# Kernel optimization log

Measured on AMD Instinct MI355X. Metric: run time of the kernel, lower is better.

The kernel has to match this reference:

```python
import jax, jax.numpy as jnp
import numpy as np

NUM_HEADS = 16


def setup_inputs() -> dict:
    key = jax.random.key(0)
    ks = jax.random.split(key, 10)
    B, S, D = 2, 2048, 1024
    x = jax.random.normal(ks[0], (B, S, D), dtype=jnp.float32)
    mask = jax.random.randint(ks[1], (B, 1, 1, S), 0, 2, dtype=jnp.int32)
    scale = 1.0 / np.sqrt(D)
    wq = jax.random.normal(ks[2], (D, D), dtype=jnp.float32) * scale
    bq = jnp.zeros((D,), dtype=jnp.float32)
    wk = jax.random.normal(ks[3], (D, D), dtype=jnp.float32) * scale
    bk = jnp.zeros((D,), dtype=jnp.float32)
    wv = jax.random.normal(ks[4], (D, D), dtype=jnp.float32) * scale
    bv = jnp.zeros((D,), dtype=jnp.float32)
    wo = jax.random.normal(ks[5], (D, D), dtype=jnp.float32) * scale
    bo = jnp.zeros((D,), dtype=jnp.float32)
    return {"x": x, "mask": mask, "wq": wq, "bq": bq, "wk": wk, "bk": bk,
            "wv": wv, "bv": bv, "wo": wo, "bo": bo}


def reference(x, mask, wq, bq, wk, bk, wv, bv, wo, bo):
    B, S, D = x.shape
    H = NUM_HEADS
    dk = D // H

    def split_heads(t):
        # (B, S, D) -> (B, H, S, dk)
        return t.reshape(B, S, H, dk).transpose(0, 2, 1, 3)

    # PyTorch nn.Linear: y = x @ W^T + b
    q = split_heads(x @ wq.T + bq)
    k = split_heads(x @ wk.T + bk)
    v = split_heads(x @ wv.T + bv)

    # scaled dot-product attention with explicit score matrix (as original)
    logits = jnp.einsum('bhqd,bhkd->bhqk', q, k) / jnp.sqrt(jnp.float32(dk))
    logits = jnp.where(mask == 0, jnp.float32(-1e9), logits)
    attn_weights = jax.nn.softmax(logits, axis=-1)
    # dropout(p=0.1) is identity in eval mode (deterministic reference)
    attn = jnp.einsum('bhqk,bhkd->bhqd', attn_weights, v)

    attn = attn.transpose(0, 2, 1, 3).reshape(B, S, D)
    out = attn @ wo.T + bo
    return out, attn_weights
```

## Files before the change

kernel.cpp:

```cpp
#include <hip/hip_runtime.h>
#include <hip/hip_bf16.h>

#define DEV __device__ __forceinline__

typedef __attribute__((ext_vector_type(8))) __bf16 bf16x8;
typedef __attribute__((ext_vector_type(8))) short s16x8;
typedef __attribute__((ext_vector_type(4))) float f32x4;
typedef __attribute__((ext_vector_type(2))) unsigned long long u64x2;

DEV f32x4 mfma16(s16x8 a, s16x8 b, f32x4 c){
  return __builtin_amdgcn_mfma_f32_16x16x32_bf16(
      __builtin_bit_cast(bf16x8, a), __builtin_bit_cast(bf16x8, b), c, 0, 0, 0);
}

DEV unsigned int cvtpk(float a, float b){
  float2 t; t.x = a; t.y = b;
  __hip_bfloat162 h = __float22bfloat162_rn(t);
  unsigned int r;
  __builtin_memcpy(&r, &h, 4);
  return r;
}

DEV unsigned short f2bf(float f){
  __hip_bfloat16 h = __float2bfloat16(f);
  unsigned short r;
  __builtin_memcpy(&r, &h, 2);
  return r;
}

DEV float bf2f(unsigned short u){
  return __builtin_bit_cast(float, ((unsigned int)u) << 16);
}

DEV unsigned long long pack4(float4 v){
  return (unsigned long long)cvtpk(v.x, v.y) | ((unsigned long long)cvtpk(v.z, v.w) << 32);
}

DEV unsigned long long pack4f(float a, float b, float c, float d){
  return (unsigned long long)cvtpk(a, b) | ((unsigned long long)cvtpk(c, d) << 32);
}

DEV void async16(const void* g, void* l){
  __builtin_amdgcn_global_load_lds(
      (const __attribute__((address_space(1))) unsigned int*)g,
      (__attribute__((address_space(3))) unsigned int*)l, 16, 0, 0);
}

__global__ __launch_bounds__(256) void cvt_kernel(
    const float* __restrict__ x, const float* __restrict__ wq, const float* __restrict__ wk,
    const float* __restrict__ wv, const float* __restrict__ wo,
    const float* __restrict__ bq, const float* __restrict__ bk, const float* __restrict__ bv,
    unsigned long long* __restrict__ xb, unsigned long long* __restrict__ wqkvb,
    unsigned long long* __restrict__ wob, float4* __restrict__ bqkv)
{
  const int i = blockIdx.x * 256 + threadIdx.x;
  const int X4 = 1048576, W4 = 262144;
  if (i < X4){
    xb[i] = pack4(((const float4*)x)[i]);
  } else if (i < X4 + 3*W4){
    int j = i - X4;
    const float* src = (j < W4) ? wq : (j < 2*W4) ? wk : wv;
    int jj = (j < W4) ? j : (j < 2*W4) ? (j - W4) : (j - 2*W4);
    wqkvb[j] = pack4(((const float4*)src)[jj]);
  } else if (i < X4 + 4*W4){
    int j = i - X4 - 3*W4;
    wob[j] = pack4(((const float4*)wo)[j]);
  } else if (i < X4 + 4*W4 + 768){
    int j = i - X4 - 4*W4;
    const float* src = (j < 256) ? bq : (j < 512) ? bk : bv;
    int jj = (j < 256) ? j : (j < 512) ? (j - 256) : (j - 512);
    bqkv[j] = ((const float4*)src)[jj];
  }
}

__global__ __launch_bounds__(512, 2) void gemm_qkv(
    const unsigned short* __restrict__ A,
    const unsigned short* __restrict__ B,
    const float* __restrict__ bias,
    unsigned short* __restrict__ oq,
    unsigned short* __restrict__ okk,
    unsigned short* __restrict__ ovt)
{
  __shared__ __align__(16) char smem[49152];
  char* As = smem;
  char* Bs = smem + 32768;
  const int tid = threadIdx.x;
  const int l = tid & 63, w = tid >> 6, g = l >> 4;

  const int orig = blockIdx.x;
  const int lin = (orig & 7) * 48 + (orig >> 3);
  const int m0 = (lin / 24) * 256, n0 = (lin % 24) * 128;
  const int rowbytes = 2048;

  f32x4 acc[4][4] = {};
  const int wr = w >> 1, wc = w & 1;
  const int wm = wr * 64, wn = wc * 64;

  const int srow = w * 8 + (l >> 3);
  const int scol = (((l & 7) ^ (l >> 3)) << 4);
  const char* Abp = (const char*)A + (size_t)(m0 + srow) * rowbytes + scol;
  const char* Bbp = (const char*)B + (size_t)(n0 + srow) * rowbytes + scol;

  int aoff[4][2], boff[4][2];
  for (int f = 0; f < 4; ++f)
    for (int ks = 0; ks < 2; ++ks){
      int ra = wm + f * 16 + (l & 15);
      aoff[f][ks] = ra * 128 + ((ks * 64 + g * 16) ^ ((l & 7) << 4));
      int rb = wn + f * 16 + (l & 15);
      boff[f][ks] = rb * 128 + ((ks * 64 + g * 16) ^ ((l & 7) << 4));
    }

  for (int kt = 0; kt < 16; ++kt){
    const char* ab = Abp + kt * 128;
    const char* bb = Bbp + kt * 128;
    for (int r = 0; r < 4; ++r)
      async16(ab + (size_t)r * 64 * rowbytes, As + r * 8192 + w * 1024);
    for (int r = 0; r < 2; ++r)
      async16(bb + (size_t)r * 64 * rowbytes, Bs + r * 8192 + w * 1024);
    __syncthreads();
    for (int ks = 0; ks < 2; ++ks){
      s16x8 af[4], bf[4];
      for (int mf = 0; mf < 4; ++mf) af[mf] = *(const s16x8*)(As + aoff[mf][ks]);
      for (int nf = 0; nf < 4; ++nf) bf[nf] = *(const s16x8*)(Bs + boff[nf][ks]);
      for (int mf = 0; mf < 4; ++mf)
        for (int nf = 0; nf < 4; ++nf)
          acc[mf][nf] = mfma16(af[mf], bf[nf], acc[mf][nf]);
    }
    __syncthreads();
  }

  if (n0 >= 2048){
    const int b2 = m0 >> 11, s0 = m0 & 2047;
    for (int h2 = 0; h2 < 2; ++h2){
      if (wr >> 1 == h2){
        for (int nf = 0; nf < 4; ++nf){
          int nloc = wn + nf * 16 + (l & 15);
          float bs = bias[n0 + nloc];
          for (int mf = 0; mf < 4; ++mf){
            int mby = ((wr & 1) * 64 + mf * 16 + g * 4) * 2;
            unsigned long long pk = pack4f(acc[mf][nf][0] + bs, acc[mf][nf][1] + bs,
                                           acc[mf][nf][2] + bs, acc[mf][nf][3] + bs);
            *(unsigned long long*)(As + nloc * 256 + (mby ^ ((nloc & 15) << 4))) = pk;
          }
        }
      }
      __syncthreads();
      for (int it = 0; it < 4; ++it){
        int idx = it * 512 + tid;
        int drow = idx >> 4, c8 = (idx & 15) * 8;
        s16x8 vv = *(const s16x8*)(As + drow * 256 + ((c8 * 2) ^ ((drow & 15) << 4)));
        *(s16x8*)(ovt + (size_t)(b2 * 1024 + (n0 - 2048) + drow) * 2048 + s0 + h2 * 128 + c8) = vv;
      }
      __syncthreads();
    }
    return;
  }

  for (int mf = 0; mf < 4; ++mf)
    for (int nf = 0; nf < 4; ++nf)
      for (int r = 0; r < 4; ++r){
        int grow = m0 + wm + mf * 16 + g * 4 + r;
        int n = n0 + wn + nf * 16 + (l & 15);
        float v = acc[mf][nf][r] + bias[n];
        if (n < 1024) oq [(size_t)grow * 1024 + n]          = f2bf(v);
        else          okk[(size_t)grow * 1024 + (n - 1024)] = f2bf(v);
      }
}

__global__ __launch_bounds__(256) void gemm_out(
    const unsigned short* __restrict__ A,
    const unsigned short* __restrict__ B,
    const float* __restrict__ bias,
    float* __restrict__ of)
{
  __shared__ __align__(16) char smem[32768];
  char* As = smem;
  char* Bs = smem + 16384;
  const int tid = threadIdx.x, l = tid & 63, w = tid >> 6, g = l >> 4;
  const int orig = blockIdx.x;
  const int lin = (orig & 7) * 64 + (orig >> 3);
  const int m0 = (lin >> 4) * 128, n0 = (lin & 15) * 64;
  const int rowbytes = 2048;

  f32x4 acc[2][4] = {};
  const int wm = w * 32;

  const int scol = (((l & 7) ^ (l >> 3)) << 4);
  const char* Abp = (const char*)A + (size_t)(m0 + w * 32 + (l >> 3)) * rowbytes + scol;
  const char* Bbp = (const char*)B + (size_t)(n0 + w * 16 + (l >> 3)) * rowbytes + scol;
  char* Asw = As + w * 4096;
  char* Bsw = Bs + w * 2048;

  int aoff[2][2], boff[4][2];
  for (int ks = 0; ks < 2; ++ks){
    for (int mf = 0; mf < 2; ++mf){
      int ra = wm + mf * 16 + (l & 15);
      aoff[mf][ks] = ra * 128 + ((ks * 64 + g * 16) ^ ((l & 7) << 4));
    }
    for (int nf = 0; nf < 4; ++nf){
      int rb = nf * 16 + (l & 15);
      boff[nf][ks] = rb * 128 + ((ks * 64 + g * 16) ^ ((l & 7) << 4));
    }
  }

  for (int kt = 0; kt < 16; ++kt){
    for (int i = 0; i < 4; ++i)
      async16(Abp + kt * 128 + (size_t)i * 8 * rowbytes, Asw + i * 1024);
    for (int i = 0; i < 2; ++i)
      async16(Bbp + kt * 128 + (size_t)i * 8 * rowbytes, Bsw + i * 1024);
    __syncthreads();
    for (int ks = 0; ks < 2; ++ks){
      s16x8 af[2], bf[4];
      for (int mf = 0; mf < 2; ++mf) af[mf] = *(const s16x8*)(As + aoff[mf][ks]);
      for (int nf = 0; nf < 4; ++nf) bf[nf] = *(const s16x8*)(Bs + boff[nf][ks]);
      for (int mf = 0; mf < 2; ++mf)
        for (int nf = 0; nf < 4; ++nf)
          acc[mf][nf] = mfma16(af[mf], bf[nf], acc[mf][nf]);
    }
    __syncthreads();
  }

  __syncthreads();
  char* stg = smem + w * 8192;
  float bv4[4];
  for (int nf = 0; nf < 4; ++nf) bv4[nf] = bias[n0 + nf * 16 + (l & 15)];
  for (int mf = 0; mf < 2; ++mf)
    for (int nf = 0; nf < 4; ++nf)
      for (int r = 0; r < 4; ++r){
        int row = mf * 16 + g * 4 + r;
        int colb = (nf * 16 + (l & 15)) * 4;
        *(float*)(stg + row * 256 + (colb ^ ((row & 7) << 4))) = acc[mf][nf][r] + bv4[nf];
      }
  __syncthreads();
  for (int t = 0; t < 8; ++t){
    int row = t * 4 + (l >> 4);
    int colb = ((l & 15) * 16) ^ ((row & 7) << 4);
    f32x4 v = *(const f32x4*)(stg + row * 256 + colb);
    __builtin_nontemporal_store(v, (f32x4*)&of[(size_t)(m0 + wm + row) * 1024 + n0 + (l & 15) * 4]);
  }
}

__global__ __launch_bounds__(512) void attn_kernel(
    const unsigned short* __restrict__ qb,
    const unsigned short* __restrict__ kb,
    const unsigned short* __restrict__ vtb,
    const int* __restrict__ mask,
    float* __restrict__ Pout,
    unsigned short* __restrict__ attnb)
{
  const int flat = blockIdx.x;
  const int sw = (flat & 7) * 256 + (flat >> 3);
  const int qt = sw & 63, h = (sw >> 6) & 15, b = sw >> 10;
  const int tid = threadIdx.x, l = tid & 63, w = tid >> 6, g = l >> 4;
  const int q0 = qt * 32;

  __shared__ __align__(16) unsigned long long estu[16384];
  __shared__ float maskadd[2048];
  __shared__ float zpart[8][32];
  __shared__ float zfullinv[32];

  char* Ebase = (char*)estu;

  for (int i = tid; i < 2048; i += 512)
    maskadd[i] = mask[b * 2048 + i] ? 0.0f : -1e30f;

  s16x8 qf[2][2];
  for (int mf = 0; mf < 2; ++mf)
    for (int ks = 0; ks < 2; ++ks)
      qf[mf][ks] = *(const s16x8*)(qb + (size_t)(b*2048 + q0 + mf*16 + (l&15)) * 1024
                                   + h*64 + ks*32 + g*8);

  const unsigned short* Kb = kb + (size_t)b * 2048 * 1024 + h * 64;
  const unsigned short* Vb = vtb + ((size_t)b * 1024 + h * 64) * 2048;

  __syncthreads();

  float zacc[2] = {0.0f, 0.0f};
  for (int jj = 0; jj < 4; ++jj){
    const int kk0 = w * 256 + jj * 64;
    const int cb = kk0 * 2;
    f32x4 c[2][4] = {};
    for (int nh = 0; nh < 2; ++nh){
      s16x8 kf[2][2];
      for (int n2 = 0; n2 < 2; ++n2)
        for (int ks = 0; ks < 2; ++ks)
          kf[n2][ks] = *(const s16x8*)(Kb + (size_t)(kk0 + (nh*2+n2)*16 + (l&15)) * 1024 + ks*32 + g*8);
      __builtin_amdgcn_s_setprio(1);
      for (int ks = 0; ks < 2; ++ks)
        for (int mf = 0; mf < 2; ++mf)
          for (int n2 = 0; n2 < 2; ++n2)
            c[mf][nh*2+n2] = mfma16(kf[n2][ks], qf[mf][ks], c[mf][nh*2+n2]);
      __builtin_amdgcn_s_setprio(0);
    }
    for (int mf = 0; mf < 2; ++mf){
      int q = mf*16 + (l & 15);
      for (int nf = 0; nf < 4; ++nf){
        f32x4 ma = *(const f32x4*)&maskadd[kk0 + nf*16 + g*4];
        f32x4 e;
        for (int r = 0; r < 4; ++r){
          e[r] = __expf(fmaf(c[mf][nf][r], 0.125f, ma[r]));
          zacc[mf] += e[r];
        }
        *(unsigned long long*)(Ebase + q*4096 + cb + ((nf*32 + g*8) ^ ((q & 7) << 4))) =
            pack4f(e[0], e[1], e[2], e[3]);
      }
    }
  }
  for (int mf = 0; mf < 2; ++mf){
    float z = zacc[mf];
    z += __shfl_xor(z, 16, 64);
    z += __shfl_xor(z, 32, 64);
    zacc[mf] = z;
  }
  if (g == 0){
    zpart[w][l & 15]        = zacc[0];
    zpart[w][16 + (l & 15)] = zacc[1];
  }
  __syncthreads();
  if (tid < 32){
    float s = 0.0f;
    for (int ww = 0; ww < 8; ++ww) s += zpart[ww][tid];
    zfullinv[tid] = 1.0f / s;
  }
  __syncthreads();

  float* Pb = Pout + ((size_t)(b*16 + h) * 2048 + q0) * 2048;
  f32x4 pv[2][4] = {};
  for (int jj = 0; jj < 4; ++jj){
    const int kk0 = w * 256 + jj * 64;
    const int cb = kk0 * 2;
    s16x8 pa[2][2];
    for (int mf = 0; mf < 2; ++mf)
      for (int ks = 0; ks < 2; ++ks){
        int q = mf*16 + (l & 15);
        const unsigned long long* pp =
            (const unsigned long long*)(Ebase + q*4096 + cb + ((ks*64 + g*16) ^ ((q & 7) << 4)));
        u64x2 t; t[0] = pp[0]; t[1] = pp[1];
        pa[mf][ks] = __builtin_bit_cast(s16x8, t);
      }
    for (int dh = 0; dh < 2; ++dh){
      s16x8 vf[2][2];
      for (int d2 = 0; d2 < 2; ++d2)
        for (int ks = 0; ks < 2; ++ks)
          vf[d2][ks] = *(const s16x8*)(Vb + (size_t)((dh*2+d2)*16 + (l&15)) * 2048 + kk0 + ks*32 + g*8);
      __builtin_amdgcn_s_setprio(1);
      for (int ks = 0; ks < 2; ++ks)
        for (int mf = 0; mf < 2; ++mf)
          for (int d2 = 0; d2 < 2; ++d2)
            pv[mf][dh*2+d2] = mfma16(pa[mf][ks], vf[d2][ks], pv[mf][dh*2+d2]);
      __builtin_amdgcn_s_setprio(0);
    }
    for (int t = 0; t < 8; ++t){
      int row = t * 4 + (l >> 4);
      unsigned long long pk =
          *(const unsigned long long*)(Ebase + row*4096 + cb + (((l & 15) * 8) ^ ((row & 7) << 4)));
      float zr = zfullinv[row];
      f32x4 ps;
      ps[0] = bf2f((unsigned short)(pk      )) * zr;
      ps[1] = bf2f((unsigned short)(pk >> 16)) * zr;
      ps[2] = bf2f((unsigned short)(pk >> 32)) * zr;
      ps[3] = bf2f((unsigned short)(pk >> 48)) * zr;
      __builtin_nontemporal_store(ps, (f32x4*)&Pb[(size_t)row * 2048 + kk0 + (l & 15) * 4]);
    }
  }

  __syncthreads();
  char* bufw = Ebase + w * 8192;
  for (int mf = 0; mf < 2; ++mf)
    for (int dn = 0; dn < 4; ++dn)
      for (int r = 0; r < 4; ++r){
        int row = mf*16 + g*4 + r, col = dn*16 + (l & 15);
        *(float*)(bufw + row*256 + ((col*4) ^ (((row >> 2) & 3) << 6))) = pv[mf][dn][r];
      }
  __syncthreads();
  {
    int row = tid >> 4, c4 = (tid & 15) * 4;
    int off = row*256 + ((c4*4) ^ (((row >> 2) & 3) << 6));
    f32x4 s = {};
    for (int ww = 0; ww < 8; ++ww)
      s += *(const f32x4*)(Ebase + ww*8192 + off);
    float zr = zfullinv[row];
    unsigned long long ov = pack4f(s[0]*zr, s[1]*zr, s[2]*zr, s[3]*zr);
    *(unsigned long long*)&attnb[(size_t)(b*2048 + q0 + row) * 1024 + h*64 + c4] = ov;
  }
}

extern "C" void kernel_launch(void* const* d_in, const int* in_sizes, int n_in,
                              void* d_out, int out_size, void* d_ws, size_t ws_size,
                              hipStream_t stream)
{
  const float* x  = (const float*)d_in[0];
  const int* mask = (const int*)d_in[1];
  const float* wq = (const float*)d_in[2];
  const float* bq = (const float*)d_in[3];
  const float* wk = (const float*)d_in[4];
  const float* bk = (const float*)d_in[5];
  const float* wv = (const float*)d_in[6];
  const float* bv = (const float*)d_in[7];
  const float* wo = (const float*)d_in[8];
  const float* bo = (const float*)d_in[9];

  char* ws = (char*)d_ws;
  unsigned short* xb    = (unsigned short*)(ws);
  unsigned short* wqkvb = (unsigned short*)(ws + 8388608);
  unsigned short* wob   = (unsigned short*)(ws + 14680064);
  float*          bqkv  = (float*)(ws + 16777216);
  unsigned short* qb    = (unsigned short*)(ws + 16793600);
  unsigned short* kb    = (unsigned short*)(ws + 25182208);
  unsigned short* vtb   = (unsigned short*)(ws + 33570816);
  unsigned short* attnb = (unsigned short*)(ws + 41959424);

  float* fout = (float*)d_out;
  float* Pout = fout + 4194304;

  cvt_kernel<<<8195, 256, 0, stream>>>(x, wq, wk, wv, wo, bq, bk, bv,
                                       (unsigned long long*)xb, (unsigned long long*)wqkvb,
                                       (unsigned long long*)wob, (float4*)bqkv);
  gemm_qkv<<<384, 512, 0, stream>>>(xb, wqkvb, bqkv, qb, kb, vtb);
  attn_kernel<<<2048, 512, 0, stream>>>(qb, kb, vtb, mask, Pout, attnb);
  gemm_out<<<512, 256, 0, stream>>>(attnb, wob, bo, fout);
}
```

Baseline: 230.6 us.

## Retile output projection GEMM to 256x64 blocks with 8 waves

The output projection GEMM now uses 256x64 tiles with 512 threads and a 4x2 wave grid (64x32 per wave), instead of 128x64 tiles with 256 threads. The grid halves to 256 blocks. The larger tile reuses each B tile across more rows and cuts redundant global loads. The epilogue is rewritten to stage results through shared memory in two 128-row halves with coalesced nontemporal stores. The trade-off is fewer blocks (256 on a 256-CU part) and more shared memory per block, which may reduce latency hiding.

New measurement: 233.2 us. No clear change (+1.1%).

```diff
diff --git a/kernel.cpp b/kernel.cpp
--- a/kernel.cpp
+++ b/kernel.cpp
@@ -167,76 +167,80 @@
       }
 }
 
-__global__ __launch_bounds__(256) void gemm_out(
+__global__ __launch_bounds__(512, 2) void gemm_out(
     const unsigned short* __restrict__ A,
     const unsigned short* __restrict__ B,
     const float* __restrict__ bias,
     float* __restrict__ of)
 {
-  __shared__ __align__(16) char smem[32768];
+  __shared__ __align__(16) char smem[40960];
   char* As = smem;
-  char* Bs = smem + 16384;
+  char* Bs = smem + 32768;
   const int tid = threadIdx.x, l = tid & 63, w = tid >> 6, g = l >> 4;
   const int orig = blockIdx.x;
-  const int lin = (orig & 7) * 64 + (orig >> 3);
-  const int m0 = (lin >> 4) * 128, n0 = (lin & 15) * 64;
+  const int lin = (orig & 7) * 32 + (orig >> 3);
+  const int m0 = (lin >> 4) * 256, n0 = (lin & 15) * 64;
   const int rowbytes = 2048;
 
-  f32x4 acc[2][4] = {};
-  const int wm = w * 32;
-
+  f32x4 acc[4][2] = {};
+  const int wr = w >> 1, wc = w & 1;
+  const int wm = wr * 64, wn = wc * 32;
+
+  const int srow = w * 8 + (l >> 3);
   const int scol = (((l & 7) ^ (l >> 3)) << 4);
-  const char* Abp = (const char*)A + (size_t)(m0 + w * 32 + (l >> 3)) * rowbytes + scol;
-  const char* Bbp = (const char*)B + (size_t)(n0 + w * 16 + (l >> 3)) * rowbytes + scol;
-  char* Asw = As + w * 4096;
-  char* Bsw = Bs + w * 2048;
-
-  int aoff[2][2], boff[4][2];
+  const char* Abp = (const char*)A + (size_t)(m0 + srow) * rowbytes + scol;
+  const char* Bbp = (const char*)B + (size_t)(n0 + srow) * rowbytes + scol;
+
+  int aoff[4][2], boff[2][2];
   for (int ks = 0; ks < 2; ++ks){
-    for (int mf = 0; mf < 2; ++mf){
+    for (int mf = 0; mf < 4; ++mf){
       int ra = wm + mf * 16 + (l & 15);
       aoff[mf][ks] = ra * 128 + ((ks * 64 + g * 16) ^ ((l & 7) << 4));
     }
-    for (int nf = 0; nf < 4; ++nf){
-      int rb = nf * 16 + (l & 15);
+    for (int nf = 0; nf < 2; ++nf){
+      int rb = wn + nf * 16 + (l & 15);
       boff[nf][ks] = rb * 128 + ((ks * 64 + g * 16) ^ ((l & 7) << 4));
     }
   }
 
   for (int kt = 0; kt < 16; ++kt){
-    for (int i = 0; i < 4; ++i)
-      async16(Abp + kt * 128 + (size_t)i * 8 * rowbytes, Asw + i * 1024);
-    for (int i = 0; i < 2; ++i)
-      async16(Bbp + kt * 128 + (size_t)i * 8 * rowbytes, Bsw + i * 1024);
+    const char* ab = Abp + kt * 128;
+    for (int r = 0; r < 4; ++r)
+      async16(ab + (size_t)r * 64 * rowbytes, As + r * 8192 + w * 1024);
+    async16(Bbp + kt * 128, Bs + w * 1024);
     __syncthreads();
     for (int ks = 0; ks < 2; ++ks){
-      s16x8 af[2], bf[4];
-      for (int mf = 0; mf < 2; ++mf) af[mf] = *(const s16x8*)(As + aoff[mf][ks]);
-      for (int nf = 0; nf < 4; ++nf) bf[nf] = *(const s16x8*)(Bs + boff[nf][ks]);
-      for (int mf = 0; mf < 2; ++mf)
-        for (int nf = 0; nf < 4; ++nf)
+      s16x8 af[4], bf[2];
+      for (int mf = 0; mf < 4; ++mf) af[mf] = *(const s16x8*)(As + aoff[mf][ks]);
+      for (int nf = 0; nf < 2; ++nf) bf[nf] = *(const s16x8*)(Bs + boff[nf][ks]);
+      for (int mf = 0; mf < 4; ++mf)
+        for (int nf = 0; nf < 2; ++nf)
           acc[mf][nf] = mfma16(af[mf], bf[nf], acc[mf][nf]);
     }
     __syncthreads();
   }
 
-  __syncthreads();
-  char* stg = smem + w * 8192;
-  float bv4[4];
-  for (int nf = 0; nf < 4; ++nf) bv4[nf] = bias[n0 + nf * 16 + (l & 15)];
-  for (int mf = 0; mf < 2; ++mf)
-    for (int nf = 0; nf < 4; ++nf)
-      for (int r = 0; r < 4; ++r){
-        int row = mf * 16 + g * 4 + r;
-        int colb = (nf * 16 + (l & 15)) * 4;
-        *(float*)(stg + row * 256 + (colb ^ ((row & 7) << 4))) = acc[mf][nf][r] + bv4[nf];
-      }
-  __syncthreads();
-  for (int t = 0; t < 8; ++t){
-    int row = t * 4 + (l >> 4);
-    int colb = ((l & 15) * 16) ^ ((row & 7) << 4);
-    f32x4 v = *(const f32x4*)(stg + row * 256 + colb);
-    __builtin_nontemporal_store(v, (f32x4*)&of[(size_t)(m0 + wm + row) * 1024 + n0 + (l & 15) * 4]);
+  float bv2[2];
+  for (int nf = 0; nf < 2; ++nf) bv2[nf] = bias[n0 + wn + nf * 16 + (l & 15)];
+  for (int h2 = 0; h2 < 2; ++h2){
+    if ((wr >> 1) == h2){
+      for (int mf = 0; mf < 4; ++mf)
+        for (int nf = 0; nf < 2; ++nf)
+          for (int r = 0; r < 4; ++r){
+            int lrow = (wr & 1) * 64 + mf * 16 + g * 4 + r;
+            int colb = (wn + nf * 16 + (l & 15)) * 4;
+            *(float*)(smem + lrow * 256 + (colb ^ ((lrow & 7) << 4))) = acc[mf][nf][r] + bv2[nf];
+          }
+    }
+    __syncthreads();
+    for (int it = 0; it < 4; ++it){
+      int idx = it * 512 + tid;
+      int lrow = idx >> 4, c4 = (idx & 15) * 4;
+      f32x4 v = *(const f32x4*)(smem + lrow * 256 + ((c4 * 4) ^ ((lrow & 7) << 4)));
+      __builtin_nontemporal_store(v,
+          (f32x4*)&of[(size_t)(m0 + h2 * 128 + lrow) * 1024 + n0 + c4]);
+    }
+    __syncthreads();
   }
 }
 
@@ -418,5 +422,5 @@
                                        (unsigned long long*)wob, (float4*)bqkv);
   gemm_qkv<<<384, 512, 0, stream>>>(xb, wqkvb, bqkv, qb, kb, vtb);
   attn_kernel<<<2048, 512, 0, stream>>>(qb, kb, vtb, mask, Pout, attnb);
-  gemm_out<<<512, 256, 0, stream>>>(attnb, wob, bo, fout);
-}
+  gemm_out<<<256, 512, 0, stream>>>(attnb, wob, bo, fout);
+}
```
